# Kernel optimization log

Measured on AMD Instinct MI355X. Metric: run time of the kernel, lower is better.

The kernel has to match this reference:

```python
import jax, jax.numpy as jnp
import numpy as np

N_NODES = 100000

def _sage_conv(x, src, dst, W_l, b_l, W_r):
    # PyG SAGEConv(aggr='mean'): out = lin_l(mean_{j in N(i)} x_j) + lin_r(x_i)
    agg = jax.ops.segment_sum(x[src], dst, num_segments=N_NODES)          # [N, F]
    cnt = jax.ops.segment_sum(jnp.ones_like(dst, dtype=x.dtype), dst,
                              num_segments=N_NODES)                        # [N]
    mean = agg / jnp.maximum(cnt, 1.0)[:, None]
    return mean @ W_l + b_l + x @ W_r

def setup_inputs() -> dict:
    key = jax.random.key(0)
    ks = jax.random.split(key, 10)
    F_in, H = 128, 16
    E, P = 1600000, 2000000
    x = jax.random.normal(ks[0], (N_NODES, F_in), dtype=jnp.float32)
    edge_index = jax.random.randint(ks[1], (2, E), 0, N_NODES, dtype=jnp.int64)
    decode_index = jax.random.randint(ks[2], (2, P), 0, N_NODES, dtype=jnp.int64)
    s1 = 1.0 / np.sqrt(F_in)
    s2 = 1.0 / np.sqrt(H)
    W1l = jax.random.uniform(ks[3], (F_in, H), jnp.float32, -s1, s1)
    b1 = jax.random.uniform(ks[4], (H,), jnp.float32, -s1, s1)
    W1r = jax.random.uniform(ks[5], (F_in, H), jnp.float32, -s1, s1)
    W2l = jax.random.uniform(ks[6], (H, H), jnp.float32, -s2, s2)
    b2 = jax.random.uniform(ks[7], (H,), jnp.float32, -s2, s2)
    W2r = jax.random.uniform(ks[8], (H, H), jnp.float32, -s2, s2)
    return {"x": x, "W1l": W1l, "b1": b1, "W1r": W1r,
            "W2l": W2l, "b2": b2, "W2r": W2r,
            "edge_index": edge_index, "decode_index": decode_index}

def reference(x, W1l, b1, W1r, W2l, b2, W2r, edge_index, decode_index):
    src, dst = edge_index[0], edge_index[1]
    h = _sage_conv(x, src, dst, W1l, b1, W1r)          # conv1
    h = jax.nn.relu(h)                                  # relu (dropout: eval -> identity)
    h = _sage_conv(h, src, dst, W2l, b2, W2r)           # conv2
    logits = jnp.sum(h[decode_index[0]] * h[decode_index[1]], axis=1)  # [P]
    return jax.nn.sigmoid(logits)
```

## Files before the change

kernel.cpp:

```cpp
#include <hip/hip_runtime.h>
#include <hip/hip_fp16.h>

#define N_NODES 100000
#define F_IN 128
#define H 16
#define NBIN 391
#define BINCAP 4608
#define ECHUNK 4096
#define QSCALE 4096.0f
#define QINV (1.0f / 4096.0f)

__device__ inline unsigned int packi16(float a, float b) {
  int ia = __float2int_rn(fminf(fmaxf(a * QSCALE, -32767.f), 32767.f));
  int ib = __float2int_rn(fminf(fmaxf(b * QSCALE, -32767.f), 32767.f));
  return (unsigned int)((ia & 0xffff) | (ib << 16));
}

__global__ void __launch_bounds__(512) k_init(int* __restrict__ binCur) {
  int t = threadIdx.x;
  if (t < NBIN) binCur[t] = t * BINCAP;
}

__global__ void __launch_bounds__(256) k_lin1(
    const float* __restrict__ x, const float* __restrict__ W1l,
    const float* __restrict__ W1r, unsigned short* __restrict__ y1l,
    float* __restrict__ y1r) {
  __shared__ float red[2 * H * 128];
  int t = threadIdx.x;
  int part = __builtin_amdgcn_readfirstlane(t >> 7);
  int ln = t & 127;
  int n = blockIdx.x * 128 + ln;
  int nc = (n < N_NODES) ? n : (N_NODES - 1);
  const float4* xr = (const float4*)(x + (size_t)nc * F_IN + part * (F_IN / 2));
  float4 xv[16];
#pragma unroll
  for (int j = 0; j < 16; ++j) xv[j] = xr[j];
  const float* Wl = W1l + part * (F_IN / 2) * H;
  const float* Wr = W1r + part * (F_IN / 2) * H;
  float al[H], ar[H];
#pragma unroll
  for (int c = 0; c < H; ++c) { al[c] = 0.f; ar[c] = 0.f; }
#pragma unroll
  for (int j = 0; j < 16; ++j) {
    float xs[4] = {xv[j].x, xv[j].y, xv[j].z, xv[j].w};
#pragma unroll
    for (int jj = 0; jj < 4; ++jj) {
      int k = j * 4 + jj;
#pragma unroll
      for (int c = 0; c < H; ++c) {
        al[c] = fmaf(xs[jj], Wl[k * H + c], al[c]);
        ar[c] = fmaf(xs[jj], Wr[k * H + c], ar[c]);
      }
    }
  }
  if (part == 1) {
#pragma unroll
    for (int c = 0; c < H; ++c) {
      red[c * 128 + ln] = al[c];
      red[(H + c) * 128 + ln] = ar[c];
    }
  }
  __syncthreads();
  if (part == 0 && n < N_NODES) {
#pragma unroll
    for (int c = 0; c < H; ++c) {
      al[c] += red[c * 128 + ln];
      ar[c] += red[(H + c) * 128 + ln];
    }
    uint4 w0, w1;
    w0.x = packi16(al[0], al[1]);  w0.y = packi16(al[2], al[3]);
    w0.z = packi16(al[4], al[5]);  w0.w = packi16(al[6], al[7]);
    w1.x = packi16(al[8], al[9]);  w1.y = packi16(al[10], al[11]);
    w1.z = packi16(al[12], al[13]); w1.w = packi16(al[14], al[15]);
    uint4* ol = (uint4*)(y1l + (size_t)n * H);
    ol[0] = w0;
    ol[1] = w1;
    float4* orr = (float4*)(y1r + (size_t)n * H);
#pragma unroll
    for (int q = 0; q < 4; ++q)
      orr[q] = make_float4(ar[4 * q], ar[4 * q + 1], ar[4 * q + 2], ar[4 * q + 3]);
  }
}

__global__ void __launch_bounds__(512) k_binfill(
    const int* __restrict__ src, const int* __restrict__ dst,
    int* __restrict__ binCur, int* __restrict__ recs, int E) {
  __shared__ int hist[512];
  __shared__ int gbase[512];
  __shared__ int cnt2[512];
  int t = threadIdx.x;
  hist[t] = 0;
  cnt2[t] = 0;
  __syncthreads();
  int base = blockIdx.x * ECHUNK;
  int rec[8], bin[8];
#pragma unroll
  for (int j = 0; j < 8; ++j) {
    int e = base + j * 512 + t;
    if (e < E) {
      int s = src[e];
      int d = dst[e];
      rec[j] = (s << 8) | (d & 255);
      bin[j] = d >> 8;
      atomicAdd(&hist[bin[j]], 1);
    } else {
      bin[j] = -1;
    }
  }
  __syncthreads();
  if (t < NBIN) {
    int c = hist[t];
    gbase[t] = (c > 0) ? atomicAdd(&binCur[t], c) : 0;
  }
  __syncthreads();
#pragma unroll
  for (int j = 0; j < 8; ++j) {
    if (bin[j] >= 0) {
      int loc = atomicAdd(&cnt2[bin[j]], 1);
      int slot = gbase[bin[j]] + loc;
      if (slot < (bin[j] + 1) * BINCAP)
        recs[slot] = rec[j];
    }
  }
}

__global__ void __launch_bounds__(512) k_group(
    int* __restrict__ recs, const int* __restrict__ binCur,
    int* __restrict__ deg, int* __restrict__ rowBeg) {
  __shared__ int lrec[BINCAP];
  __shared__ int hist[256];
  __shared__ int off[256];
  __shared__ int cur[256];
  int t = threadIdx.x;
  int b = blockIdx.x;
  int rbase = b * BINCAP;
  int R = binCur[b] - rbase;
  if (R > BINCAP) R = BINCAP;
  if (t < 256) hist[t] = 0;
  __syncthreads();
#pragma unroll
  for (int j = 0; j < 9; ++j) {
    int idx = j * 512 + t;
    if (idx < R) {
      int r = recs[rbase + idx];
      lrec[idx] = r;
      atomicAdd(&hist[r & 255], 1);
    }
  }
  __syncthreads();
  if (t < 256) off[t] = hist[t];
  __syncthreads();
  for (int o = 1; o < 256; o <<= 1) {
    int u = 0;
    if (t < 256 && t >= o) u = off[t - o];
    __syncthreads();
    if (t < 256) off[t] += u;
    __syncthreads();
  }
  if (t < 256) {
    int ex = off[t] - hist[t];
    cur[t] = ex;
    int n = (b << 8) + t;
    if (n < N_NODES) {
      deg[n] = hist[t];
      rowBeg[n] = rbase + ex;
    }
  }
  __syncthreads();
#pragma unroll
  for (int j = 0; j < 9; ++j) {
    int idx = j * 512 + t;
    if (idx < R) {
      int r = lrec[idx];
      int slot = atomicAdd(&cur[r & 255], 1);
      recs[rbase + slot] = r >> 8;
    }
  }
}

__global__ void __launch_bounds__(256) k_gather1(
    const int* __restrict__ srcSorted, const int* __restrict__ deg,
    const int* __restrict__ rowBeg, const unsigned short* __restrict__ y1l,
    const float* __restrict__ y1r, const float* __restrict__ b1,
    const float* __restrict__ W2l, const float* __restrict__ W2r,
    unsigned short* __restrict__ z2l, float* __restrict__ z2r) {
  int tid = blockIdx.x * 256 + threadIdx.x;
  int n = tid >> 2;
  int q = tid & 3;
  if (n >= N_NODES) return;
  int beg = rowBeg[n];
  int dg = deg[n];
  int end = beg + dg;
  int acc0 = 0, acc1 = 0, acc2 = 0, acc3 = 0;
  int i = beg;
  for (; i + 4 <= end; i += 4) {
    int sq = srcSorted[i + q];
#pragma unroll
    for (int j = 0; j < 4; ++j) {
      int sj = __shfl(sq, j, 4);
      uint2 v = *(const uint2*)(y1l + (size_t)sj * H + q * 4);
      acc0 += ((int)(v.x << 16)) >> 16;
      acc1 += ((int)v.x) >> 16;
      acc2 += ((int)(v.y << 16)) >> 16;
      acc3 += ((int)v.y) >> 16;
    }
  }
  for (; i < end; ++i) {
    int sj = srcSorted[i];
    uint2 v = *(const uint2*)(y1l + (size_t)sj * H + q * 4);
    acc0 += ((int)(v.x << 16)) >> 16;
    acc1 += ((int)v.x) >> 16;
    acc2 += ((int)(v.y << 16)) >> 16;
    acc3 += ((int)v.y) >> 16;
  }
  float s = (1.f / fmaxf((float)dg, 1.f)) * QINV;
  float4 yr = *(const float4*)(y1r + (size_t)n * H + q * 4);
  float4 bb = *(const float4*)(b1 + q * 4);
  float h1x = fmaxf(fmaf((float)acc0, s, bb.x + yr.x), 0.f);
  float h1y = fmaxf(fmaf((float)acc1, s, bb.y + yr.y), 0.f);
  float h1z = fmaxf(fmaf((float)acc2, s, bb.z + yr.z), 0.f);
  float h1w = fmaxf(fmaf((float)acc3, s, bb.w + yr.w), 0.f);
  float zl0 = 0.f, zl1 = 0.f, zl2 = 0.f, zl3 = 0.f;
  float zr0 = 0.f, zr1 = 0.f, zr2 = 0.f, zr3 = 0.f;
#pragma unroll
  for (int sl = 0; sl < 4; ++sl) {
    float hx = __shfl(h1x, sl, 4);
    float hy = __shfl(h1y, sl, 4);
    float hz = __shfl(h1z, sl, 4);
    float hw = __shfl(h1w, sl, 4);
    float hk4[4] = {hx, hy, hz, hw};
#pragma unroll
    for (int j = 0; j < 4; ++j) {
      int k = sl * 4 + j;
      float4 wl = *(const float4*)(W2l + k * H + q * 4);
      float4 wr = *(const float4*)(W2r + k * H + q * 4);
      float hk = hk4[j];
      zl0 = fmaf(hk, wl.x, zl0); zl1 = fmaf(hk, wl.y, zl1);
      zl2 = fmaf(hk, wl.z, zl2); zl3 = fmaf(hk, wl.w, zl3);
      zr0 = fmaf(hk, wr.x, zr0); zr1 = fmaf(hk, wr.y, zr1);
      zr2 = fmaf(hk, wr.z, zr2); zr3 = fmaf(hk, wr.w, zr3);
    }
  }
  uint2 pk;
  pk.x = packi16(zl0, zl1);
  pk.y = packi16(zl2, zl3);
  *(uint2*)(z2l + (size_t)n * H + q * 4) = pk;
  *(float4*)(z2r + (size_t)n * H + q * 4) = make_float4(zr0, zr1, zr2, zr3);
}

__global__ void __launch_bounds__(256) k_gather2(
    const int* __restrict__ srcSorted, const int* __restrict__ deg,
    const int* __restrict__ rowBeg, const unsigned short* __restrict__ z2l,
    const float* __restrict__ z2r, const float* __restrict__ b2,
    __half* __restrict__ h2) {
  int tid = blockIdx.x * 256 + threadIdx.x;
  int n = tid >> 2;
  int q = tid & 3;
  if (n >= N_NODES) return;
  int beg = rowBeg[n];
  int dg = deg[n];
  int end = beg + dg;
  int acc0 = 0, acc1 = 0, acc2 = 0, acc3 = 0;
  int i = beg;
  for (; i + 4 <= end; i += 4) {
    int sq = srcSorted[i + q];
#pragma unroll
    for (int j = 0; j < 4; ++j) {
      int sj = __shfl(sq, j, 4);
      uint2 v = *(const uint2*)(z2l + (size_t)sj * H + q * 4);
      acc0 += ((int)(v.x << 16)) >> 16;
      acc1 += ((int)v.x) >> 16;
      acc2 += ((int)(v.y << 16)) >> 16;
      acc3 += ((int)v.y) >> 16;
    }
  }
  for (; i < end; ++i) {
    int sj = srcSorted[i];
    uint2 v = *(const uint2*)(z2l + (size_t)sj * H + q * 4);
    acc0 += ((int)(v.x << 16)) >> 16;
    acc1 += ((int)v.x) >> 16;
    acc2 += ((int)(v.y << 16)) >> 16;
    acc3 += ((int)v.y) >> 16;
  }
  float s = (1.f / fmaxf((float)dg, 1.f)) * QINV;
  float4 zr = *(const float4*)(z2r + (size_t)n * H + q * 4);
  float4 bb = *(const float4*)(b2 + q * 4);
  float v0 = fmaf((float)acc0, s, bb.x + zr.x);
  float v1 = fmaf((float)acc1, s, bb.y + zr.y);
  float v2 = fmaf((float)acc2, s, bb.z + zr.z);
  float v3 = fmaf((float)acc3, s, bb.w + zr.w);
  __half2 h0 = __floats2half2_rn(v0, v1);
  __half2 h1 = __floats2half2_rn(v2, v3);
  uint2 pk;
  pk.x = *(unsigned int*)&h0;
  pk.y = *(unsigned int*)&h1;
  *(uint2*)(h2 + (size_t)n * H + q * 4) = pk;
}

__device__ inline float dot8h(uint4 u, uint4 v) {
  float acc = 0.f;
  const unsigned int* uw = (const unsigned int*)&u;
  const unsigned int* vw = (const unsigned int*)&v;
#pragma unroll
  for (int j = 0; j < 4; ++j) {
    float2 a = __half22float2(*(const __half2*)&uw[j]);
    float2 b = __half22float2(*(const __half2*)&vw[j]);
    acc = fmaf(a.x, b.x, acc);
    acc = fmaf(a.y, b.y, acc);
  }
  return acc;
}

__global__ void __launch_bounds__(256) k_decode(
    const int* __restrict__ ps, const int* __restrict__ pd,
    const __half* __restrict__ h2, float* __restrict__ out, int P) {
  int p = blockIdx.x * 256 + threadIdx.x;
  if (p >= P) return;
  int a = ps[p];
  int b = pd[p];
  const uint4* ha = (const uint4*)(h2 + (size_t)a * H);
  const uint4* hb = (const uint4*)(h2 + (size_t)b * H);
  uint4 u0 = ha[0], u1 = ha[1];
  uint4 v0 = hb[0], v1 = hb[1];
  float acc = dot8h(u0, v0) + dot8h(u1, v1);
  out[p] = 1.f / (1.f + __expf(-acc));
}

extern "C" void kernel_launch(void* const* d_in, const int* in_sizes, int n_in,
                              void* d_out, int out_size, void* d_ws, size_t ws_size,
                              hipStream_t stream) {
  const float* x   = (const float*)d_in[0];
  const float* W1l = (const float*)d_in[1];
  const float* b1  = (const float*)d_in[2];
  const float* W1r = (const float*)d_in[3];
  const float* W2l = (const float*)d_in[4];
  const float* b2  = (const float*)d_in[5];
  const float* W2r = (const float*)d_in[6];
  const int* ei = (const int*)d_in[7];
  const int* di = (const int*)d_in[8];
  const int E = in_sizes[7] / 2;
  const int P = in_sizes[8] / 2;

  const size_t NF = (size_t)N_NODES * H;
  unsigned short* y1l = (unsigned short*)d_ws;
  __half*         h2  = (__half*)y1l;
  unsigned short* z2l = y1l + NF;
  float*  y1r = (float*)(z2l + NF);
  float*  z2r = y1r;
  int* recs   = (int*)(y1r + NF);
  int* binCur = recs + (size_t)NBIN * BINCAP;
  int* deg    = binCur + 512;
  int* rowBeg = deg + N_NODES;

  const int lin1Blocks = (N_NODES + 127) / 128;
  const int fillBlocks = (E + ECHUNK - 1) / ECHUNK;
  const int gatherBlocks = ((N_NODES * 4) + 255) / 256;

  k_init<<<1, 512, 0, stream>>>(binCur);
  k_lin1<<<lin1Blocks, 256, 0, stream>>>(x, W1l, W1r, y1l, y1r);
  k_binfill<<<fillBlocks, 512, 0, stream>>>(ei, ei + E, binCur, recs, E);
  k_group<<<NBIN, 512, 0, stream>>>(recs, binCur, deg, rowBeg);
  k_gather1<<<gatherBlocks, 256, 0, stream>>>(recs, deg, rowBeg, y1l, y1r,
                                              b1, W2l, W2r, z2l, z2r);
  k_gather2<<<gatherBlocks, 256, 0, stream>>>(recs, deg, rowBeg, z2l, z2r,
                                              b2, h2);
  k_decode<<<(P + 255) / 256, 256, 0, stream>>>(di, di + P, h2, (float*)d_out, P);
}
```

Before: 225.4 us.

## Merge lin1 and edge binning into one launch, unroll gathers and decode

Folds the dense first-layer linear kernel and the edge bin-fill kernel into a single heterogeneous launch, with block index choosing the role, so both run concurrently and one launch is saved. Bin-fill now uses 256-thread blocks with half-size chunks. The two gather kernels gain an 8-edge unrolled loop that issues two independent row loads per step to raise memory-level parallelism. The decode kernel processes two pairs per thread with vectorized index loads and a float2 store. In exchange there are more bin-fill blocks hitting the global bin cursors with atomics, and higher register pressure in the unrolled loops.

```diff
diff --git a/kernel.cpp b/kernel.cpp
--- a/kernel.cpp
+++ b/kernel.cpp
@@ -6,7 +6,8 @@
 #define H 16
 #define NBIN 391
 #define BINCAP 4608
-#define ECHUNK 4096
+#define ECHUNK 2048
+#define LIN1B 782
 #define QSCALE 4096.0f
 #define QINV (1.0f / 4096.0f)
 
@@ -21,105 +22,105 @@
   if (t < NBIN) binCur[t] = t * BINCAP;
 }
 
-__global__ void __launch_bounds__(256) k_lin1(
+__global__ void __launch_bounds__(256) k_front(
     const float* __restrict__ x, const float* __restrict__ W1l,
     const float* __restrict__ W1r, unsigned short* __restrict__ y1l,
-    float* __restrict__ y1r) {
-  __shared__ float red[2 * H * 128];
+    float* __restrict__ y1r, const int* __restrict__ src,
+    const int* __restrict__ dst, int* __restrict__ binCur,
+    int* __restrict__ recs, int E) {
+  __shared__ float smem[2 * H * 128];
   int t = threadIdx.x;
-  int part = __builtin_amdgcn_readfirstlane(t >> 7);
-  int ln = t & 127;
-  int n = blockIdx.x * 128 + ln;
-  int nc = (n < N_NODES) ? n : (N_NODES - 1);
-  const float4* xr = (const float4*)(x + (size_t)nc * F_IN + part * (F_IN / 2));
-  float4 xv[16];
-#pragma unroll
-  for (int j = 0; j < 16; ++j) xv[j] = xr[j];
-  const float* Wl = W1l + part * (F_IN / 2) * H;
-  const float* Wr = W1r + part * (F_IN / 2) * H;
-  float al[H], ar[H];
-#pragma unroll
-  for (int c = 0; c < H; ++c) { al[c] = 0.f; ar[c] = 0.f; }
-#pragma unroll
-  for (int j = 0; j < 16; ++j) {
-    float xs[4] = {xv[j].x, xv[j].y, xv[j].z, xv[j].w};
-#pragma unroll
-    for (int jj = 0; jj < 4; ++jj) {
-      int k = j * 4 + jj;
+  if (blockIdx.x < LIN1B) {
+    float* red = smem;
+    int part = __builtin_amdgcn_readfirstlane(t >> 7);
+    int ln = t & 127;
+    int n = blockIdx.x * 128 + ln;
+    int nc = (n < N_NODES) ? n : (N_NODES - 1);
+    const float4* xr = (const float4*)(x + (size_t)nc * F_IN + part * (F_IN / 2));
+    float4 xv[16];
+#pragma unroll
+    for (int j = 0; j < 16; ++j) xv[j] = xr[j];
+    const float* Wl = W1l + part * (F_IN / 2) * H;
+    const float* Wr = W1r + part * (F_IN / 2) * H;
+    float al[H], ar[H];
+#pragma unroll
+    for (int c = 0; c < H; ++c) { al[c] = 0.f; ar[c] = 0.f; }
+#pragma unroll
+    for (int j = 0; j < 16; ++j) {
+      float xs[4] = {xv[j].x, xv[j].y, xv[j].z, xv[j].w};
+#pragma unroll
+      for (int jj = 0; jj < 4; ++jj) {
+        int k = j * 4 + jj;
+#pragma unroll
+        for (int c = 0; c < H; ++c) {
+          al[c] = fmaf(xs[jj], Wl[k * H + c], al[c]);
+          ar[c] = fmaf(xs[jj], Wr[k * H + c], ar[c]);
+        }
+      }
+    }
+    if (part == 1) {
 #pragma unroll
       for (int c = 0; c < H; ++c) {
-        al[c] = fmaf(xs[jj], Wl[k * H + c], al[c]);
-        ar[c] = fmaf(xs[jj], Wr[k * H + c], ar[c]);
+        red[c * 128 + ln] = al[c];
+        red[(H + c) * 128 + ln] = ar[c];
       }
     }
-  }
-  if (part == 1) {
-#pragma unroll
-    for (int c = 0; c < H; ++c) {
-      red[c * 128 + ln] = al[c];
-      red[(H + c) * 128 + ln] = ar[c];
-    }
-  }
-  __syncthreads();
-  if (part == 0 && n < N_NODES) {
-#pragma unroll
-    for (int c = 0; c < H; ++c) {
-      al[c] += red[c * 128 + ln];
-      ar[c] += red[(H + c) * 128 + ln];
-    }
-    uint4 w0, w1;
-    w0.x = packi16(al[0], al[1]);  w0.y = packi16(al[2], al[3]);
-    w0.z = packi16(al[4], al[5]);  w0.w = packi16(al[6], al[7]);
-    w1.x = packi16(al[8], al[9]);  w1.y = packi16(al[10], al[11]);
-    w1.z = packi16(al[12], al[13]); w1.w = packi16(al[14], al[15]);
-    uint4* ol = (uint4*)(y1l + (size_t)n * H);
-    ol[0] = w0;
-    ol[1] = w1;
-    float4* orr = (float4*)(y1r + (size_t)n * H);
-#pragma unroll
-    for (int q = 0; q < 4; ++q)
-      orr[q] = make_float4(ar[4 * q], ar[4 * q + 1], ar[4 * q + 2], ar[4 * q + 3]);
-  }
-}
-
-__global__ void __launch_bounds__(512) k_binfill(
-    const int* __restrict__ src, const int* __restrict__ dst,
-    int* __restrict__ binCur, int* __restrict__ recs, int E) {
-  __shared__ int hist[512];
-  __shared__ int gbase[512];
-  __shared__ int cnt2[512];
-  int t = threadIdx.x;
-  hist[t] = 0;
-  cnt2[t] = 0;
-  __syncthreads();
-  int base = blockIdx.x * ECHUNK;
-  int rec[8], bin[8];
-#pragma unroll
-  for (int j = 0; j < 8; ++j) {
-    int e = base + j * 512 + t;
-    if (e < E) {
-      int s = src[e];
-      int d = dst[e];
-      rec[j] = (s << 8) | (d & 255);
-      bin[j] = d >> 8;
-      atomicAdd(&hist[bin[j]], 1);
-    } else {
-      bin[j] = -1;
-    }
-  }
-  __syncthreads();
-  if (t < NBIN) {
-    int c = hist[t];
-    gbase[t] = (c > 0) ? atomicAdd(&binCur[t], c) : 0;
-  }
-  __syncthreads();
-#pragma unroll
-  for (int j = 0; j < 8; ++j) {
-    if (bin[j] >= 0) {
-      int loc = atomicAdd(&cnt2[bin[j]], 1);
-      int slot = gbase[bin[j]] + loc;
-      if (slot < (bin[j] + 1) * BINCAP)
-        recs[slot] = rec[j];
+    __syncthreads();
+    if (part == 0 && n < N_NODES) {
+#pragma unroll
+      for (int c = 0; c < H; ++c) {
+        al[c] += red[c * 128 + ln];
+        ar[c] += red[(H + c) * 128 + ln];
+      }
+      uint4 w0, w1;
+      w0.x = packi16(al[0], al[1]);  w0.y = packi16(al[2], al[3]);
+      w0.z = packi16(al[4], al[5]);  w0.w = packi16(al[6], al[7]);
+      w1.x = packi16(al[8], al[9]);  w1.y = packi16(al[10], al[11]);
+      w1.z = packi16(al[12], al[13]); w1.w = packi16(al[14], al[15]);
+      uint4* ol = (uint4*)(y1l + (size_t)n * H);
+      ol[0] = w0;
+      ol[1] = w1;
+      float4* orr = (float4*)(y1r + (size_t)n * H);
+#pragma unroll
+      for (int q = 0; q < 4; ++q)
+        orr[q] = make_float4(ar[4 * q], ar[4 * q + 1], ar[4 * q + 2], ar[4 * q + 3]);
+    }
+  } else {
+    int* hist = (int*)smem;
+    int* gbase = hist + 512;
+    int* cnt2 = gbase + 512;
+    hist[t] = 0; hist[256 + t] = 0;
+    cnt2[t] = 0; cnt2[256 + t] = 0;
+    __syncthreads();
+    int base = (blockIdx.x - LIN1B) * ECHUNK;
+    int rec[8], bin[8];
+#pragma unroll
+    for (int j = 0; j < 8; ++j) {
+      int e = base + j * 256 + t;
+      if (e < E) {
+        int s = src[e];
+        int d = dst[e];
+        rec[j] = (s << 8) | (d & 255);
+        bin[j] = d >> 8;
+        atomicAdd(&hist[bin[j]], 1);
+      } else {
+        bin[j] = -1;
+      }
+    }
+    __syncthreads();
+    for (int u = t; u < NBIN; u += 256) {
+      int c = hist[u];
+      gbase[u] = (c > 0) ? atomicAdd(&binCur[u], c) : 0;
+    }
+    __syncthreads();
+#pragma unroll
+    for (int j = 0; j < 8; ++j) {
+      if (bin[j] >= 0) {
+        int loc = atomicAdd(&cnt2[bin[j]], 1);
+        int slot = gbase[bin[j]] + loc;
+        if (slot < (bin[j] + 1) * BINCAP)
+          recs[slot] = rec[j];
+      }
     }
   }
 }
@@ -193,6 +194,21 @@
   int end = beg + dg;
   int acc0 = 0, acc1 = 0, acc2 = 0, acc3 = 0;
   int i = beg;
+  for (; i + 8 <= end; i += 8) {
+    int sqa = srcSorted[i + q];
+    int sqb = srcSorted[i + 4 + q];
+#pragma unroll
+    for (int j = 0; j < 4; ++j) {
+      int sa = __shfl(sqa, j, 4);
+      int sb = __shfl(sqb, j, 4);
+      uint2 va = *(const uint2*)(y1l + (size_t)sa * H + q * 4);
+      uint2 vb = *(const uint2*)(y1l + (size_t)sb * H + q * 4);
+      acc0 += (((int)(va.x << 16)) >> 16) + (((int)(vb.x << 16)) >> 16);
+      acc1 += (((int)va.x) >> 16) + (((int)vb.x) >> 16);
+      acc2 += (((int)(va.y << 16)) >> 16) + (((int)(vb.y << 16)) >> 16);
+      acc3 += (((int)va.y) >> 16) + (((int)vb.y) >> 16);
+    }
+  }
   for (; i + 4 <= end; i += 4) {
     int sq = srcSorted[i + q];
 #pragma unroll
@@ -262,6 +278,21 @@
   int end = beg + dg;
   int acc0 = 0, acc1 = 0, acc2 = 0, acc3 = 0;
   int i = beg;
+  for (; i + 8 <= end; i += 8) {
+    int sqa = srcSorted[i + q];
+    int sqb = srcSorted[i + 4 + q];
+#pragma unroll
+    for (int j = 0; j < 4; ++j) {
+      int sa = __shfl(sqa, j, 4);
+      int sb = __shfl(sqb, j, 4);
+      uint2 va = *(const uint2*)(z2l + (size_t)sa * H + q * 4);
+      uint2 vb = *(const uint2*)(z2l + (size_t)sb * H + q * 4);
+      acc0 += (((int)(va.x << 16)) >> 16) + (((int)(vb.x << 16)) >> 16);
+      acc1 += (((int)va.x) >> 16) + (((int)vb.x) >> 16);
+      acc2 += (((int)(va.y << 16)) >> 16) + (((int)(vb.y << 16)) >> 16);
+      acc3 += (((int)va.y) >> 16) + (((int)vb.y) >> 16);
+    }
+  }
   for (; i + 4 <= end; i += 4) {
     int sq = srcSorted[i + q];
 #pragma unroll
@@ -314,16 +345,28 @@
 __global__ void __launch_bounds__(256) k_decode(
     const int* __restrict__ ps, const int* __restrict__ pd,
     const __half* __restrict__ h2, float* __restrict__ out, int P) {
-  int p = blockIdx.x * 256 + threadIdx.x;
+  int t = blockIdx.x * 256 + threadIdx.x;
+  int p = t * 2;
   if (p >= P) return;
-  int a = ps[p];
-  int b = pd[p];
-  const uint4* ha = (const uint4*)(h2 + (size_t)a * H);
-  const uint4* hb = (const uint4*)(h2 + (size_t)b * H);
-  uint4 u0 = ha[0], u1 = ha[1];
-  uint4 v0 = hb[0], v1 = hb[1];
-  float acc = dot8h(u0, v0) + dot8h(u1, v1);
-  out[p] = 1.f / (1.f + __expf(-acc));
+  int2 av = *(const int2*)(ps + p);
+  int2 bv = *(const int2*)(pd + p);
+  const uint4* ha0 = (const uint4*)(h2 + (size_t)av.x * H);
+  const uint4* hb0 = (const uint4*)(h2 + (size_t)bv.x * H);
+  const uint4* ha1 = (const uint4*)(h2 + (size_t)av.y * H);
+  const uint4* hb1 = (const uint4*)(h2 + (size_t)bv.y * H);
+  uint4 u00 = ha0[0], u01 = ha0[1];
+  uint4 v00 = hb0[0], v01 = hb0[1];
+  uint4 u10 = ha1[0], u11 = ha1[1];
+  uint4 v10 = hb1[0], v11 = hb1[1];
+  float d0 = dot8h(u00, v00) + dot8h(u01, v01);
+  float d1 = dot8h(u10, v10) + dot8h(u11, v11);
+  float o0 = 1.f / (1.f + __expf(-d0));
+  float o1 = 1.f / (1.f + __expf(-d1));
+  if (p + 1 < P) {
+    *(float2*)(out + p) = make_float2(o0, o1);
+  } else {
+    out[p] = o0;
+  }
 }
 
 extern "C" void kernel_launch(void* const* d_in, const int* in_sizes, int n_in,
@@ -352,17 +395,18 @@
   int* deg    = binCur + 512;
   int* rowBeg = deg + N_NODES;
 
-  const int lin1Blocks = (N_NODES + 127) / 128;
   const int fillBlocks = (E + ECHUNK - 1) / ECHUNK;
+  const int frontBlocks = LIN1B + fillBlocks;
   const int gatherBlocks = ((N_NODES * 4) + 255) / 256;
+  const int decodeBlocks = ((P + 1) / 2 + 255) / 256;
 
   k_init<<<1, 512, 0, stream>>>(binCur);
-  k_lin1<<<lin1Blocks, 256, 0, stream>>>(x, W1l, W1r, y1l, y1r);
-  k_binfill<<<fillBlocks, 512, 0, stream>>>(ei, ei + E, binCur, recs, E);
+  k_front<<<frontBlocks, 256, 0, stream>>>(x, W1l, W1r, y1l, y1r,
+                                           ei, ei + E, binCur, recs, E);
   k_group<<<NBIN, 512, 0, stream>>>(recs, binCur, deg, rowBeg);
   k_gather1<<<gatherBlocks, 256, 0, stream>>>(recs, deg, rowBeg, y1l, y1r,
                                               b1, W2l, W2r, z2l, z2r);
   k_gather2<<<gatherBlocks, 256, 0, stream>>>(recs, deg, rowBeg, z2l, z2r,
                                               b2, h2);
-  k_decode<<<(P + 255) / 256, 256, 0, stream>>>(di, di + P, h2, (float*)d_out, P);
-}
+  k_decode<<<decodeBlocks, 256, 0, stream>>>(di, di + P, h2, (float*)d_out, P);
+}
```

Measured after the change: 225.5 us. No clear change (+0.0%).
